# Kernel tuning notes

Hardware: AMD Instinct MI355X
Metric: run time of the kernel (lower is better)

Reference implementation:

```python
import jax, jax.numpy as jnp
import numpy as np

B, H, W, D, L, M = 16, 256, 256, 32, 4, 12  # batch, grid H, grid W, d_model, num_layers, modes
BN_EPS = 1e-5


def setup_inputs() -> dict:
    key = jax.random.key(0)
    ks = jax.random.split(key, 12)
    scale = 1.0 / (D * D)  # SpectralConv2d init scale: 1/(in_ch*out_ch)
    return {
        "x": jax.random.normal(ks[0], (B, H, W), jnp.float32),
        "coords_x": jax.random.uniform(ks[1], (1, 2, 1, H, W), dtype=jnp.float32),
        # linear_in: 3 -> D
        "w_in": jax.random.normal(ks[2], (D, 3), jnp.float32) * 0.3,
        "b_in": jnp.zeros((D,), jnp.float32),
        # per-layer spectral weights (real/imag), torch.rand-style uniform [0,1)*scale
        "w1r": jax.random.uniform(ks[3], (L, D, D, M, M), dtype=jnp.float32) * scale,
        "w1i": jax.random.uniform(ks[4], (L, D, D, M, M), dtype=jnp.float32) * scale,
        "w2r": jax.random.uniform(ks[5], (L, D, D, M, M), dtype=jnp.float32) * scale,
        "w2i": jax.random.uniform(ks[6], (L, D, D, M, M), dtype=jnp.float32) * scale,
        # per-layer pointwise linear D -> D
        "lw": jax.random.normal(ks[7], (L, D, D), jnp.float32) * (1.0 / np.sqrt(D)),
        "lb": jnp.zeros((L, D), jnp.float32),
        # per-layer BatchNorm affine params
        "gamma": jnp.ones((L, D), jnp.float32),
        "beta": jnp.zeros((L, D), jnp.float32),
        # linear_out: D -> 1
        "w_out": jax.random.normal(ks[8], (1, D), jnp.float32) * (1.0 / np.sqrt(D)),
        "b_out": jnp.zeros((1,), jnp.float32),
    }


def _fourier_layer(h, w1, w2, lw, lb, gamma, beta):
    # h: [B, D, H, W]
    Bh, C, Hh, Wh = h.shape
    h_ft = jnp.fft.rfft2(h)  # [B, D, H, W//2+1] complex64
    # low-mode truncation + complex channel mixing on two corner blocks
    top = jnp.einsum('bixy,ioxy->boxy', h_ft[:, :, :M, :M], w1)
    bot = jnp.einsum('bixy,ioxy->boxy', h_ft[:, :, Hh - M:, :M], w2)
    out_ft = jnp.zeros((Bh, C, Hh, Wh // 2 + 1), jnp.complex64)
    out_ft = out_ft.at[:, :, :M, :M].set(top).at[:, :, Hh - M:, :M].set(bot)
    y = jnp.fft.irfft2(out_ft, s=(Hh, Wh))  # [B, D, H, W]
    # residual pointwise linear (x + Linear(x)), then ReLU, then BatchNorm2d (batch stats)
    y = y + jnp.einsum('bchw,oc->bohw', y, lw) + lb[None, :, None, None]
    y = jax.nn.relu(y)
    mean = y.mean(axis=(0, 2, 3), keepdims=True)
    var = y.var(axis=(0, 2, 3), keepdims=True)
    y = (y - mean) * jax.lax.rsqrt(var + BN_EPS)
    return y * gamma[None, :, None, None] + beta[None, :, None, None]


def reference(x, coords_x, w_in, b_in, w1r, w1i, w2r, w2i, lw, lb, gamma, beta, w_out, b_out):
    # coords_x: [1,2,1,H,W] -> squeeze dim 2 -> broadcast to [B,2,H,W]
    cx = jnp.broadcast_to(coords_x[:, :, 0], (x.shape[0], 2, H, W))
    h = jnp.concatenate([x[:, None], cx], axis=1)  # [B, 3, H, W]
    h = jnp.einsum('bchw,dc->bdhw', h, w_in) + b_in[None, :, None, None]  # linear_in
    for i in range(L):  # fixed small layer count
        h = _fourier_layer(h, w1r[i] + 1j * w1i[i], w2r[i] + 1j * w2i[i],
                           lw[i], lb[i], gamma[i], beta[i])
    out = jnp.einsum('bdhw,od->bohw', h, w_out) + b_out[None, :, None, None]  # linear_out
    return out[:, 0]  # [B, H, W]
```

## Files before the change

kernel.cpp:

```cpp
#include <hip/hip_runtime.h>

constexpr double PI2 = 6.283185307179586476925286766559;
constexpr float INV_HW = 1.0f / 65536.0f;


__global__ __launch_bounds__(256) void k_init(float* __restrict__ cs,
                                              float* __restrict__ Tg) {
  int t = threadIdx.x;
  double a = PI2 * (double)t / 256.0;
  cs[2*t]   = (float)cos(a);
  cs[2*t+1] = (float)sin(a);
  for (int i = t; i < 1536; i += 256) {
    int k = i >> 7, xs = i & 127;
    double ang = PI2 * (double)(k * xs) / 256.0;
    Tg[i]        = (float)cos(ang);
    Tg[1536 + i] = (float)sin(ang);
  }
}

__global__ __launch_bounds__(256) void k_prep(
    const float* __restrict__ w1r, const float* __restrict__ w1i,
    const float* __restrict__ w2r, const float* __restrict__ w2i,
    const float* __restrict__ lw, float* __restrict__ wf)
{
  const int bid = blockIdx.x;
  const int l = bid / 288, m = bid % 288;
  const int ky = m / 12, kx = m % 12;
  const int kyp = (ky < 12) ? ky : ky - 12;
  const float* wr_ = ((ky < 12) ? w1r : w2r) + l*147456;
  const float* wi_ = ((ky < 12) ? w1i : w2i) + l*147456;
  __shared__ float wre[1024], wim[1024], lwl[1024];
  const int tid = threadIdx.x;
  for (int f = tid; f < 1024; f += 256) {
    int idx = f*144 + kyp*12 + kx;
    wre[f] = wr_[idx]; wim[f] = wi_[idx];
    lwl[f] = lw[l*1024 + f];
  }
  __syncthreads();
  float* o_ = wf + (long)bid*2048;
  for (int f = tid; f < 1024; f += 256) {
    int i = f >> 5, o = f & 31;
    float ar = wre[f], ai = wim[f];
    #pragma unroll
    for (int c = 0; c < 32; ++c) {
      float lv = lwl[o*32 + c];
      ar += wre[i*32 + c] * lv;
      ai += wim[i*32 + c] * lv;
    }
    o_[f] = ar; o_[1024 + f] = ai;
  }
}

__global__ __launch_bounds__(256) void k_embed_fwd(
    const float* __restrict__ xin, const float* __restrict__ coords,
    const float* __restrict__ w_in, const float* __restrict__ b_in,
    const float* __restrict__ cs, float* __restrict__ gxo)
{
  __shared__ float wl[96], bl[32];
  __shared__ __align__(16) float csl[512];
  __shared__ float S[32*257];
  const int tid = threadIdx.x;
  if (tid < 96) wl[tid] = w_in[tid];
  if (tid >= 96 && tid < 128) bl[tid-96] = b_in[tid-96];
  for (int f = tid; f < 512; f += 256) csl[f] = cs[f];
  const int b = blockIdx.x >> 8, y = blockIdx.x & 255;
  const float xv = xin[(b*256 + y)*256 + tid];
  const float c0 = coords[y*256 + tid];
  const float c1 = coords[65536 + y*256 + tid];
  __syncthreads();
  #pragma unroll 8
  for (int d = 0; d < 32; ++d)
    S[d*257 + tid] = wl[3*d]*xv + wl[3*d+1]*c0 + wl[3*d+2]*c1 + bl[d];
  __syncthreads();
  const int task = tid >> 5, o = tid & 31;
  if (task < 6) {
    const int kx0 = task*2, kx1 = kx0 + 1;
    const float* Sp = &S[o*257];
    const float s0v = Sp[0], s128 = Sp[128];
    float ar0 = s0v + s128, ai0 = 0.f;
    float ar1 = s0v - s128, ai1 = 0.f;
    int t0 = kx0, t1 = kx1;
    for (int xx = 1; xx < 128; ++xx) {
      float a = Sp[xx], bv = Sp[256 - xx];
      float e = a + bv, od = a - bv;
      float2 w0 = *(const float2*)&csl[2*t0];
      float2 w1 = *(const float2*)&csl[2*t1];
      ar0 += e*w0.x;  ai0 -= od*w0.y;
      ar1 += e*w1.x;  ai1 -= od*w1.y;
      t0 = (t0 + kx0) & 255;
      t1 = (t1 + kx1) & 255;
    }
    float4 w4; w4.x = ar0; w4.y = ai0; w4.z = ar1; w4.w = ai1;
    *(float4*)(gxo + ((long)(b*256 + y)*32 + o)*24 + task*4) = w4;
  }
}

__global__ __launch_bounds__(512) void k_spec(
    const float* __restrict__ gx, const float* __restrict__ cs,
    const float* __restrict__ bnp, const float* __restrict__ wfl,
    float* __restrict__ gy)
{
  const int bid = (blockIdx.x % 8) * 24 + blockIdx.x / 8;
  const int b = bid / 12, kx = bid % 12;
  __shared__ float2 Z[32*257];
  __shared__ float fcl[24*66];
  __shared__ float fml[24*66];
  __shared__ __align__(16) float csl[512];
  const int tid = threadIdx.x;
  if (tid < 512) csl[tid] = cs[tid];
  {
    const int ch = tid & 31;
    float sc = 1.0f, badd = 0.0f;
    if (bnp) { sc = bnp[ch]; if (kx == 0) badd = 256.0f * bnp[32 + ch]; }
    const float* src = gx + ((long)(b*256)*32 + ch)*24 + 2*kx;
    const int ybase = tid >> 5;
    #pragma unroll
    for (int i = 0; i < 16; ++i) {
      int y = ybase + 16*i;
      float2 v = *(const float2*)(src + (long)y*768);
      float2 w; w.x = sc*v.x + badd; w.y = sc*v.y;
      Z[ch*257 + y] = w;
    }
  }
  __syncthreads();
  for (int t = tid; t < 832; t += 512) {
    const int hf = t & 1, r = t >> 1;
    const int pr = r % 13, ch = r / 13;
    const int kyv = (pr <= 10) ? (pr + 1) : ((pr == 11) ? 0 : 244);
    const int y0 = hf << 7;
    int tt = (kyv * y0) & 255;
    float A = 0.f, Bv = 0.f, C2 = 0.f, D = 0.f;
    const float2* Zp = &Z[ch*257 + y0];
    for (int i = 0; i < 128; ++i) {
      float2 v = Zp[i];
      float2 w = *(const float2*)&csl[2*tt];
      A  += v.x*w.x;  D  += v.x*w.y;
      C2 += v.y*w.x;  Bv += v.y*w.y;
      tt = (tt + kyv) & 255;
    }
    A  += __shfl_xor(A, 1, 64);
    Bv += __shfl_xor(Bv, 1, 64);
    C2 += __shfl_xor(C2, 1, 64);
    D  += __shfl_xor(D, 1, 64);
    if (hf == 0) {
      const int slo = (pr <= 10) ? (pr + 1) : ((pr == 11) ? 0 : 12);
      fcl[slo*66 + 2*ch]     = A + Bv;
      fcl[slo*66 + 2*ch + 1] = C2 - D;
      if (pr <= 10) {
        fcl[(23 - pr)*66 + 2*ch]     = A - Bv;
        fcl[(23 - pr)*66 + 2*ch + 1] = C2 + D;
      }
    }
  }
  __syncthreads();
  for (int t = tid; t < 768; t += 512) {
    const int ky = t >> 5, o = t & 31;
    const float* wb = wfl + ((long)(ky*12 + kx))*2048;
    const float* fr = &fcl[ky*66];
    float ar = 0.f, ai = 0.f;
    #pragma unroll
    for (int i = 0; i < 32; ++i) {
      float fre = fr[2*i], fim = fr[2*i+1];
      float wr = wb[i*32 + o], wi = wb[1024 + i*32 + o];
      ar += fre*wr - fim*wi;
      ai += fre*wi + fim*wr;
    }
    fml[ky*66 + 2*o]     = ar;
    fml[ky*66 + 2*o + 1] = ai;
  }
  __syncthreads();
  {
    const int yp = tid & 127, og = tid >> 7;
    float tc[24], tsn[24];
    #pragma unroll
    for (int s = 0; s < 24; ++s) {
      int kyv = (s < 12) ? s : (232 + s);
      int tt = (kyv * yp) & 255;
      tc[s] = csl[2*tt]; tsn[s] = csl[2*tt+1];
    }
    const int yhi = (256 - yp) & 255;
    float* rowLo = gy + ((long)(b*256 + yp))*768 + kx*64;
    float* rowHi = gy + ((long)(b*256 + yhi))*768 + kx*64;
    #pragma unroll
    for (int oo = 0; oo < 8; oo += 2) {
      const int o = og*8 + oo;
      float A1a=0.f,A2a=0.f,A3a=0.f,A4a=0.f;
      float A1b=0.f,A2b=0.f,A3b=0.f,A4b=0.f;
      #pragma unroll
      for (int s = 0; s < 24; ++s) {
        float fra = fml[s*66 + 2*o],     fia = fml[s*66 + 2*o + 1];
        float frb = fml[s*66 + 2*o + 2], fib = fml[s*66 + 2*o + 3];
        float c = tc[s], sn = tsn[s];
        A1a += fra*c;  A2a += fia*sn;  A3a += fra*sn;  A4a += fia*c;
        A1b += frb*c;  A2b += fib*sn;  A3b += frb*sn;  A4b += fib*c;
      }
      float4 lo, hi;
      lo.x = (A1a - A2a)*INV_HW; lo.y = (A3a + A4a)*INV_HW;
      lo.z = (A1b - A2b)*INV_HW; lo.w = (A3b + A4b)*INV_HW;
      hi.x = (A1a + A2a)*INV_HW; hi.y = (A4a - A3a)*INV_HW;
      hi.z = (A1b + A2b)*INV_HW; hi.w = (A4b - A3b)*INV_HW;
      *(float4*)(rowLo + 2*o) = lo;
      *(float4*)(rowHi + 2*o) = hi;
    }
  }
  if (tid < 32) {
    const int o = tid;
    float re = 0.f, im = 0.f;
    #pragma unroll
    for (int s = 0; s < 24; ++s) {
      float fr = fml[s*66 + 2*o], fi = fml[s*66 + 2*o + 1];
      if (s & 1) { re -= fr; im -= fi; } else { re += fr; im += fi; }
    }
    float* row = gy + ((long)(b*256 + 128))*768 + kx*64;
    row[2*o]     = re*INV_HW;
    row[2*o + 1] = im*INV_HW;
  }
}

__global__ __launch_bounds__(256) void k_fuse(
    const float* __restrict__ gy, const float* __restrict__ Tg,
    const float* __restrict__ lb,
    float* __restrict__ gxo, float* __restrict__ part, float* __restrict__ z)
{
  const int b = blockIdx.x >> 8, y = blockIdx.x & 255;
  const int tid = threadIdx.x;
  __shared__ __align__(16) float T[3168];
  __shared__ __align__(16) float E[32*132];
  __shared__ __align__(16) float O[32*132];
  for (int i = tid; i < 1536; i += 256) {
    int k = i >> 7, xs0 = i & 127;
    T[k*132 + xs0]        = Tg[i];
    T[1584 + k*132 + xs0] = Tg[1536 + i];
  }
  __syncthreads();
  const int xs = tid & 127, half = tid >> 7;
  const int cbase = half << 4;
  const int xhi = (256 - xs) & 255;
  float tc[12], tsn[12];
  #pragma unroll
  for (int kx = 1; kx < 12; ++kx) {
    tc[kx]  = 2.0f * T[kx*132 + xs];
    tsn[kx] = 2.0f * T[1584 + kx*132 + xs];
  }
  const float* Gg = gy + (long)(b*256 + y)*768;
  float zlo[16], zhi[16];
  #pragma unroll
  for (int cc = 0; cc < 16; cc += 2) {
    const int c = cbase + cc;
    float base0 = Gg[2*c], base1 = Gg[2*c + 2];
    float cos0 = 0.f, sin0 = 0.f, cos1 = 0.f, sin1 = 0.f;
    #pragma unroll
    for (int kx = 1; kx < 12; ++kx) {
      float4 g = *(const float4*)(Gg + kx*64 + 2*c);
      cos0 += g.x*tc[kx];  sin0 += g.y*tsn[kx];
      cos1 += g.z*tc[kx];  sin1 += g.w*tsn[kx];
    }
    const float l0 = lb[c], l1 = lb[c+1];
    zlo[cc]   = fmaxf(base0 + cos0 - sin0 + l0, 0.f);
    zhi[cc]   = fmaxf(base0 + cos0 + sin0 + l0, 0.f);
    zlo[cc+1] = fmaxf(base1 + cos1 - sin1 + l1, 0.f);
    zhi[cc+1] = fmaxf(base1 + cos1 + sin1 + l1, 0.f);
  }
  #pragma unroll
  for (int cc = 0; cc < 16; ++cc) {
    float e = (xs == 0) ? zlo[cc] : (zlo[cc] + zhi[cc]);
    float o = (xs == 0) ? 0.f     : (zlo[cc] - zhi[cc]);
    E[(cbase+cc)*132 + xs] = e;
    O[(cbase+cc)*132 + xs] = o;
  }
  if (z) {
    #pragma unroll
    for (int cc = 0; cc < 16; ++cc) {
      z[((b*32 + cbase+cc)*256 + y)*256 + xs]  = zlo[cc];
      z[((b*32 + cbase+cc)*256 + y)*256 + xhi] = zhi[cc];
    }
  }
  if (tid < 32) {
    const int c = tid;
    float acc = Gg[2*c] + lb[c];
    #pragma unroll
    for (int kx = 1; kx < 12; ++kx) {
      float2 g = *(const float2*)(Gg + kx*64 + 2*c);
      acc += (kx & 1) ? (-2.0f * g.x) : (2.0f * g.x);
    }
    float zv = fmaxf(acc, 0.f);
    E[c*132 + 128] = zv;
    if (z) z[((b*32 + c)*256 + y)*256 + 128] = zv;
  }
  __syncthreads();
  const int ch = tid & 31, seg = tid >> 5;
  float ar[12], ai[12], sq = 0.f;
  #pragma unroll
  for (int k = 0; k < 12; ++k) { ar[k] = 0.f; ai[k] = 0.f; }
  {
    const float* Erow = &E[ch*132 + seg*16];
    const float* Orow = &O[ch*132 + seg*16];
    if (gxo) {
      #pragma unroll
      for (int c4 = 0; c4 < 4; ++c4) {
        float4 E4 = *(const float4*)(Erow + 4*c4);
        float4 O4 = *(const float4*)(Orow + 4*c4);
        ar[0] += E4.x + E4.y + E4.z + E4.w;
        #pragma unroll
        for (int k = 1; k < 12; ++k) {
          float4 Tc4 = *(const float4*)&T[k*132 + seg*16 + 4*c4];
          float4 Ts4 = *(const float4*)&T[1584 + k*132 + seg*16 + 4*c4];
          ar[k] += E4.x*Tc4.x + E4.y*Tc4.y + E4.z*Tc4.z + E4.w*Tc4.w;
          ai[k] -= O4.x*Ts4.x + O4.y*Ts4.y + O4.z*Ts4.z + O4.w*Ts4.w;
        }
        sq += E4.x*E4.x + E4.y*E4.y + E4.z*E4.z + E4.w*E4.w
            + O4.x*O4.x + O4.y*O4.y + O4.z*O4.z + O4.w*O4.w;
      }
    } else {
      #pragma unroll
      for (int c4 = 0; c4 < 4; ++c4) {
        float4 E4 = *(const float4*)(Erow + 4*c4);
        float4 O4 = *(const float4*)(Orow + 4*c4);
        ar[0] += E4.x + E4.y + E4.z + E4.w;
        sq += E4.x*E4.x + E4.y*E4.y + E4.z*E4.z + E4.w*E4.w
            + O4.x*O4.x + O4.y*O4.y + O4.z*O4.z + O4.w*O4.w;
      }
    }
  }
  #pragma unroll
  for (int k = 0; k < 12; ++k) ar[k] += __shfl_xor(ar[k], 32, 64);
  #pragma unroll
  for (int k = 1; k < 12; ++k) ai[k] += __shfl_xor(ai[k], 32, 64);
  sq += __shfl_xor(sq, 32, 64);
  __syncthreads();
  float* red = O;
  const int wv = tid >> 6;
  if ((tid & 63) < 32) {
    float* r = &red[(wv*32 + ch)*25];
    #pragma unroll
    for (int k = 0; k < 12; ++k) r[k] = ar[k];
    #pragma unroll
    for (int k = 1; k < 12; ++k) r[11 + k] = ai[k];
    r[23] = sq;
  }
  __syncthreads();
  {
    const int q = tid >> 5;
    const float e0   = E[ch*132];
    const float e128 = E[ch*132 + 128];
    float* gp = gxo ? (gxo + ((long)(b*256 + y)*32 + ch)*24) : nullptr;
    #pragma unroll
    for (int j = 0; j < 3; ++j) {
      const int v = 3*q + j;
      float s = red[ch*25 + v]        + red[(32+ch)*25 + v]
              + red[(64+ch)*25 + v]   + red[(96+ch)*25 + v];
      if (v < 12) {
        s += (v & 1) ? -e128 : e128;
        if (gp) {
          gp[2*v] = s;
          if (v == 0) gp[1] = 0.f;
        }
        if (v == 0) part[(long)blockIdx.x*64 + 2*ch] = s;
      } else if (v < 23) {
        if (gp) gp[2*(v - 11) + 1] = s;
      } else {
        part[(long)blockIdx.x*64 + 2*ch + 1] = 0.5f*s + 0.5f*e0*e0 + e128*e128;
      }
    }
  }
}

__global__ __launch_bounds__(256) void k_stats(
    const float* __restrict__ part, const float* __restrict__ gamma,
    const float* __restrict__ beta, float* __restrict__ bn)
{
  const int c = blockIdx.x, tid = threadIdx.x;
  float s1 = 0.f, s2 = 0.f;
  for (int j = tid; j < 4096; j += 256) {
    s1 += part[(long)j*64 + 2*c];
    s2 += part[(long)j*64 + 2*c + 1];
  }
  #pragma unroll
  for (int d = 32; d; d >>= 1) {
    s1 += __shfl_xor(s1, d, 64);
    s2 += __shfl_xor(s2, d, 64);
  }
  __shared__ float r1[4], r2[4];
  int w = tid >> 6;
  if ((tid & 63) == 0) { r1[w] = s1; r2[w] = s2; }
  __syncthreads();
  if (tid == 0) {
    float S1 = r1[0]+r1[1]+r1[2]+r1[3];
    float S2 = r2[0]+r2[1]+r2[2]+r2[3];
    const float N = 1048576.0f;
    float mean = S1 / N;
    float var  = S2 / N - mean*mean;
    float inv  = rsqrtf(var + 1e-5f);
    float sc   = gamma[c] * inv;
    bn[c]      = sc;
    bn[32 + c] = beta[c] - mean*sc;
  }
}

__global__ __launch_bounds__(256) void k_out(
    const float* __restrict__ z, const float* __restrict__ bn,
    const float* __restrict__ w_out, const float* __restrict__ b_out,
    float* __restrict__ out)
{
  __shared__ float a[32];
  __shared__ float c0s;
  const int tid = threadIdx.x;
  if (tid < 32) a[tid] = bn[tid] * w_out[tid];
  if (tid == 0) {
    float t = b_out[0];
    for (int c = 0; c < 32; ++c) t += bn[32 + c] * w_out[c];
    c0s = t;
  }
  __syncthreads();
  int gid = blockIdx.x*256 + tid;
  int b = gid >> 14, pos = (gid & 16383) << 2;
  const float* zb = z + (long)b*2097152 + pos;
  float c0 = c0s;
  float r0 = c0, r1 = c0, r2 = c0, r3 = c0;
  #pragma unroll 8
  for (int c = 0; c < 32; ++c) {
    float4 v = *(const float4*)(zb + c*65536);
    float ac = a[c];
    r0 += v.x*ac; r1 += v.y*ac; r2 += v.z*ac; r3 += v.w*ac;
  }
  float4 res; res.x = r0; res.y = r1; res.z = r2; res.w = r3;
  *(float4*)(out + (long)b*65536 + pos) = res;
}

extern "C" void kernel_launch(void* const* d_in, const int* in_sizes, int n_in,
                              void* d_out, int out_size, void* d_ws, size_t ws_size,
                              hipStream_t stream) {
  const float* x      = (const float*)d_in[0];
  const float* coords = (const float*)d_in[1];
  const float* w_in   = (const float*)d_in[2];
  const float* b_in   = (const float*)d_in[3];
  const float* w1r    = (const float*)d_in[4];
  const float* w1i    = (const float*)d_in[5];
  const float* w2r    = (const float*)d_in[6];
  const float* w2i    = (const float*)d_in[7];
  const float* lw     = (const float*)d_in[8];
  const float* lb     = (const float*)d_in[9];
  const float* gamma  = (const float*)d_in[10];
  const float* beta   = (const float*)d_in[11];
  const float* w_out  = (const float*)d_in[12];
  const float* b_out  = (const float*)d_in[13];
  float* out = (float*)d_out;
  float* ws  = (float*)d_ws;

  float* cs   = ws;
  float* z    = cs + 512;
  float* gx   = z;
  float* wf   = z + 3145728;
  float* gy   = z + 33554432;
  float* part = gy + 3145728;
  float* Tg   = part + 294912;
  float* bn   = Tg + 294912;

  k_init<<<1, 256, 0, stream>>>(cs, Tg);
  k_prep<<<1152, 256, 0, stream>>>(w1r, w1i, w2r, w2i, lw, wf);
  k_embed_fwd<<<4096, 256, 0, stream>>>(x, coords, w_in, b_in, cs, gx);

  for (int l = 0; l < 4; ++l) {
    k_spec<<<192, 512, 0, stream>>>(gx, cs, (l == 0) ? nullptr : bn,
                                    wf + (long)l*589824, gy);
    k_fuse<<<4096, 256, 0, stream>>>(gy, Tg, lb + l*32,
                                     (l < 3) ? gx : nullptr, part,
                                     (l == 3) ? z : nullptr);
    k_stats<<<32, 256, 0, stream>>>(part, gamma + l*32, beta + l*32, bn);
  }

  k_out<<<1024, 256, 0, stream>>>(z, bn, w_out, b_out, out);
}
```

Measured before the change: 538.2 us.

## Remap fuse/embed row DFT so each wave reduces fully via shuffles, drop LDS twiddles

The thread-to-work mapping in k_fuse's partial row DFT changes so each wavefront owns 8 channels across all 8 segments. Reductions then finish with xor shuffles instead of a shared-memory scratch pass and two barriers. Twiddles are read straight from global Tg instead of being staged into LDS, which drops a staging loop, a barrier and 12.6 KB of shared memory per block. k_embed_fwd is rewritten to reuse the same even/odd folding and matrix-style DFT instead of a serial per-thread loop. The trade-offs are uncoalesced or broadcast global/L1 reads for twiddles and more shuffle instructions.

Result: slower. 619.8 us (+15.2%).

```diff
diff --git a/kernel.cpp b/kernel.cpp
--- a/kernel.cpp
+++ b/kernel.cpp
@@ -54,44 +54,90 @@
 __global__ __launch_bounds__(256) void k_embed_fwd(
     const float* __restrict__ xin, const float* __restrict__ coords,
     const float* __restrict__ w_in, const float* __restrict__ b_in,
-    const float* __restrict__ cs, float* __restrict__ gxo)
+    const float* __restrict__ Tg, float* __restrict__ gxo)
 {
   __shared__ float wl[96], bl[32];
-  __shared__ __align__(16) float csl[512];
-  __shared__ float S[32*257];
+  __shared__ __align__(16) float E[32*132];
+  __shared__ __align__(16) float O[32*132];
   const int tid = threadIdx.x;
   if (tid < 96) wl[tid] = w_in[tid];
   if (tid >= 96 && tid < 128) bl[tid-96] = b_in[tid-96];
-  for (int f = tid; f < 512; f += 256) csl[f] = cs[f];
   const int b = blockIdx.x >> 8, y = blockIdx.x & 255;
-  const float xv = xin[(b*256 + y)*256 + tid];
-  const float c0 = coords[y*256 + tid];
-  const float c1 = coords[65536 + y*256 + tid];
-  __syncthreads();
-  #pragma unroll 8
-  for (int d = 0; d < 32; ++d)
-    S[d*257 + tid] = wl[3*d]*xv + wl[3*d+1]*c0 + wl[3*d+2]*c1 + bl[d];
-  __syncthreads();
-  const int task = tid >> 5, o = tid & 31;
-  if (task < 6) {
-    const int kx0 = task*2, kx1 = kx0 + 1;
-    const float* Sp = &S[o*257];
-    const float s0v = Sp[0], s128 = Sp[128];
-    float ar0 = s0v + s128, ai0 = 0.f;
-    float ar1 = s0v - s128, ai1 = 0.f;
-    int t0 = kx0, t1 = kx1;
-    for (int xx = 1; xx < 128; ++xx) {
-      float a = Sp[xx], bv = Sp[256 - xx];
-      float e = a + bv, od = a - bv;
-      float2 w0 = *(const float2*)&csl[2*t0];
-      float2 w1 = *(const float2*)&csl[2*t1];
-      ar0 += e*w0.x;  ai0 -= od*w0.y;
-      ar1 += e*w1.x;  ai1 -= od*w1.y;
-      t0 = (t0 + kx0) & 255;
-      t1 = (t1 + kx1) & 255;
-    }
-    float4 w4; w4.x = ar0; w4.y = ai0; w4.z = ar1; w4.w = ai1;
-    *(float4*)(gxo + ((long)(b*256 + y)*32 + o)*24 + task*4) = w4;
+  const int xs = tid & 127, half = tid >> 7;
+  const int cbase = half << 4;
+  const int xhi = (256 - xs) & 255;
+  const float xvL = xin[(b*256 + y)*256 + xs];
+  const float c0L = coords[y*256 + xs];
+  const float c1L = coords[65536 + y*256 + xs];
+  const float xvH = xin[(b*256 + y)*256 + xhi];
+  const float c0H = coords[y*256 + xhi];
+  const float c1H = coords[65536 + y*256 + xhi];
+  __syncthreads();
+  #pragma unroll
+  for (int cc = 0; cc < 16; ++cc) {
+    const int c = cbase + cc;
+    float lo = wl[3*c]*xvL + wl[3*c+1]*c0L + wl[3*c+2]*c1L + bl[c];
+    float hi = wl[3*c]*xvH + wl[3*c+1]*c0H + wl[3*c+2]*c1H + bl[c];
+    E[c*132 + xs] = (xs == 0) ? lo : (lo + hi);
+    O[c*132 + xs] = (xs == 0) ? 0.f : (lo - hi);
+  }
+  if (tid < 32) {
+    const int c = tid;
+    const float xv = xin[(b*256 + y)*256 + 128];
+    const float c0 = coords[y*256 + 128];
+    const float c1 = coords[65536 + y*256 + 128];
+    E[c*132 + 128] = wl[3*c]*xv + wl[3*c+1]*c0 + wl[3*c+2]*c1 + bl[c];
+  }
+  __syncthreads();
+  const int wv = tid >> 6, lane = tid & 63;
+  const int seg = lane >> 3, chl = lane & 7;
+  const int ch = wv*8 + chl;
+  float ar[12], ai[12];
+  #pragma unroll
+  for (int k = 0; k < 12; ++k) { ar[k] = 0.f; ai[k] = 0.f; }
+  {
+    const float* Erow = &E[ch*132 + seg*16];
+    const float* Orow = &O[ch*132 + seg*16];
+    #pragma unroll
+    for (int c4 = 0; c4 < 4; ++c4) {
+      float4 E4 = *(const float4*)(Erow + 4*c4);
+      float4 O4 = *(const float4*)(Orow + 4*c4);
+      ar[0] += E4.x + E4.y + E4.z + E4.w;
+      #pragma unroll
+      for (int k = 1; k < 12; ++k) {
+        float4 Tc4 = *(const float4*)&Tg[k*128 + seg*16 + 4*c4];
+        float4 Ts4 = *(const float4*)&Tg[1536 + k*128 + seg*16 + 4*c4];
+        ar[k] += E4.x*Tc4.x + E4.y*Tc4.y + E4.z*Tc4.z + E4.w*Tc4.w;
+        ai[k] -= O4.x*Ts4.x + O4.y*Ts4.y + O4.z*Ts4.z + O4.w*Ts4.w;
+      }
+    }
+  }
+  #pragma unroll
+  for (int k = 0; k < 12; ++k) {
+    ar[k] += __shfl_xor(ar[k], 8, 64);
+    ar[k] += __shfl_xor(ar[k], 16, 64);
+    ar[k] += __shfl_xor(ar[k], 32, 64);
+  }
+  #pragma unroll
+  for (int k = 1; k < 12; ++k) {
+    ai[k] += __shfl_xor(ai[k], 8, 64);
+    ai[k] += __shfl_xor(ai[k], 16, 64);
+    ai[k] += __shfl_xor(ai[k], 32, 64);
+  }
+  {
+    const float e128 = E[ch*132 + 128];
+    float* gp = gxo + ((long)(b*256 + y)*32 + ch)*24;
+    #pragma unroll
+    for (int j = 0; j < 3; ++j) {
+      const int v = seg*3 + j;
+      if (v < 12) {
+        float s = ar[v] + ((v & 1) ? -e128 : e128);
+        gp[2*v] = s;
+        if (v == 0) gp[1] = 0.f;
+      } else if (v < 23) {
+        gp[2*(v - 11) + 1] = ai[v - 11];
+      }
+    }
   }
 }
 
@@ -224,23 +270,16 @@
 {
   const int b = blockIdx.x >> 8, y = blockIdx.x & 255;
   const int tid = threadIdx.x;
-  __shared__ __align__(16) float T[3168];
   __shared__ __align__(16) float E[32*132];
   __shared__ __align__(16) float O[32*132];
-  for (int i = tid; i < 1536; i += 256) {
-    int k = i >> 7, xs0 = i & 127;
-    T[k*132 + xs0]        = Tg[i];
-    T[1584 + k*132 + xs0] = Tg[1536 + i];
-  }
-  __syncthreads();
   const int xs = tid & 127, half = tid >> 7;
   const int cbase = half << 4;
   const int xhi = (256 - xs) & 255;
   float tc[12], tsn[12];
   #pragma unroll
   for (int kx = 1; kx < 12; ++kx) {
-    tc[kx]  = 2.0f * T[kx*132 + xs];
-    tsn[kx] = 2.0f * T[1584 + kx*132 + xs];
+    tc[kx]  = 2.0f * Tg[kx*128 + xs];
+    tsn[kx] = 2.0f * Tg[1536 + kx*128 + xs];
   }
   const float* Gg = gy + (long)(b*256 + y)*768;
   float zlo[16], zhi[16];
@@ -288,7 +327,9 @@
     if (z) z[((b*32 + c)*256 + y)*256 + 128] = zv;
   }
   __syncthreads();
-  const int ch = tid & 31, seg = tid >> 5;
+  const int wv = tid >> 6, lane = tid & 63;
+  const int seg = lane >> 3, chl = lane & 7;
+  const int ch = wv*8 + chl;
   float ar[12], ai[12], sq = 0.f;
   #pragma unroll
   for (int k = 0; k < 12; ++k) { ar[k] = 0.f; ai[k] = 0.f; }
@@ -303,8 +344,8 @@
         ar[0] += E4.x + E4.y + E4.z + E4.w;
         #pragma unroll
         for (int k = 1; k < 12; ++k) {
-          float4 Tc4 = *(const float4*)&T[k*132 + seg*16 + 4*c4];
-          float4 Ts4 = *(const float4*)&T[1584 + k*132 + seg*16 + 4*c4];
+          float4 Tc4 = *(const float4*)&Tg[k*128 + seg*16 + 4*c4];
+          float4 Ts4 = *(const float4*)&Tg[1536 + k*128 + seg*16 + 4*c4];
           ar[k] += E4.x*Tc4.x + E4.y*Tc4.y + E4.z*Tc4.z + E4.w*Tc4.w;
           ai[k] -= O4.x*Ts4.x + O4.y*Ts4.y + O4.z*Ts4.z + O4.w*Ts4.w;
         }
@@ -323,43 +364,40 @@
     }
   }
   #pragma unroll
-  for (int k = 0; k < 12; ++k) ar[k] += __shfl_xor(ar[k], 32, 64);
-  #pragma unroll
-  for (int k = 1; k < 12; ++k) ai[k] += __shfl_xor(ai[k], 32, 64);
+  for (int k = 0; k < 12; ++k) {
+    ar[k] += __shfl_xor(ar[k], 8, 64);
+    ar[k] += __shfl_xor(ar[k], 16, 64);
+    ar[k] += __shfl_xor(ar[k], 32, 64);
+  }
+  if (gxo) {
+    #pragma unroll
+    for (int k = 1; k < 12; ++k) {
+      ai[k] += __shfl_xor(ai[k], 8, 64);
+      ai[k] += __shfl_xor(ai[k], 16, 64);
+      ai[k] += __shfl_xor(ai[k], 32, 64);
+    }
+  }
+  sq += __shfl_xor(sq, 8, 64);
+  sq += __shfl_xor(sq, 16, 64);
   sq += __shfl_xor(sq, 32, 64);
-  __syncthreads();
-  float* red = O;
-  const int wv = tid >> 6;
-  if ((tid & 63) < 32) {
-    float* r = &red[(wv*32 + ch)*25];
-    #pragma unroll
-    for (int k = 0; k < 12; ++k) r[k] = ar[k];
-    #pragma unroll
-    for (int k = 1; k < 12; ++k) r[11 + k] = ai[k];
-    r[23] = sq;
-  }
-  __syncthreads();
   {
-    const int q = tid >> 5;
     const float e0   = E[ch*132];
     const float e128 = E[ch*132 + 128];
     float* gp = gxo ? (gxo + ((long)(b*256 + y)*32 + ch)*24) : nullptr;
     #pragma unroll
     for (int j = 0; j < 3; ++j) {
-      const int v = 3*q + j;
-      float s = red[ch*25 + v]        + red[(32+ch)*25 + v]
-              + red[(64+ch)*25 + v]   + red[(96+ch)*25 + v];
+      const int v = seg*3 + j;
       if (v < 12) {
-        s += (v & 1) ? -e128 : e128;
+        float s = ar[v] + ((v & 1) ? -e128 : e128);
         if (gp) {
           gp[2*v] = s;
           if (v == 0) gp[1] = 0.f;
         }
         if (v == 0) part[(long)blockIdx.x*64 + 2*ch] = s;
       } else if (v < 23) {
-        if (gp) gp[2*(v - 11) + 1] = s;
+        if (gp) gp[2*(v - 11) + 1] = ai[v - 11];
       } else {
-        part[(long)blockIdx.x*64 + 2*ch + 1] = 0.5f*s + 0.5f*e0*e0 + e128*e128;
+        part[(long)blockIdx.x*64 + 2*ch + 1] = 0.5f*sq + 0.5f*e0*e0 + e128*e128;
       }
     }
   }
@@ -458,7 +496,7 @@
 
   k_init<<<1, 256, 0, stream>>>(cs, Tg);
   k_prep<<<1152, 256, 0, stream>>>(w1r, w1i, w2r, w2i, lw, wf);
-  k_embed_fwd<<<4096, 256, 0, stream>>>(x, coords, w_in, b_in, cs, gx);
+  k_embed_fwd<<<4096, 256, 0, stream>>>(x, coords, w_in, b_in, Tg, gx);
 
   for (int l = 0; l < 4; ++l) {
     k_spec<<<192, 512, 0, stream>>>(gx, cs, (l == 0) ? nullptr : bn,
```
